# Performance work log

Hardware: AMD Instinct MI355X
Metric: run time of the kernel (lower is better)

The kernel has to match this reference:

```python
import jax, jax.numpy as jnp
import numpy as np

KH, KW = 3, 3
STRIDE = (1, 1)
PAD = (1, 1)
DIL = (1, 1)

def _unfold(x, kh, kw, stride, padding, dilation):
    # Faithful torch.nn.functional.unfold: output (B, C*kh*kw, L) with
    # feature ordering channel-slowest, then kh, then kw.
    B, C, H, W = x.shape
    h_out = (H + 2 * padding[0] - dilation[0] * (kh - 1) - 1) // stride[0] + 1
    w_out = (W + 2 * padding[1] - dilation[1] * (kw - 1) - 1) // stride[1] + 1
    xp = jnp.pad(x, ((0, 0), (0, 0), (padding[0], padding[0]), (padding[1], padding[1])))
    rows = []
    for i in range(kh):  # small fixed kernel loop (9 slices), not a data-dim loop
        for j in range(kw):
            r0 = i * dilation[0]
            c0 = j * dilation[1]
            patch = xp[:, :, r0:r0 + h_out * stride[0]:stride[0],
                             c0:c0 + w_out * stride[1]:stride[1]]  # (B,C,h_out,w_out)
            rows.append(patch)
    # stack -> (B, C, kh*kw, h_out, w_out); reorder so feature dim = C*kh*kw
    p = jnp.stack(rows, axis=2)
    p = p.reshape(B, C * kh * kw, h_out * w_out)
    return p, h_out, w_out

def transform_transposed_unfolded_input(inp_unf):
    # Default hook: identity (as in the base class).
    return inp_unf

def reference(x, weight, bias):
    B = x.shape[0]
    O = weight.shape[0]
    inp_unf, h_out, w_out = _unfold(x, KH, KW, STRIDE, PAD, DIL)   # (B, C*k*k, L)
    inp_t = jnp.swapaxes(inp_unf, 1, 2)                            # (B, L, C*k*k)
    inp_t = transform_transposed_unfolded_input(inp_t)
    w2d = weight.reshape(O, -1)                                    # (O, C*k*k)
    out_unf = jnp.einsum('blk,ok->bol', inp_t, w2d)                # (B, O, L)
    out = out_unf.reshape(B, O, h_out, w_out)
    out = out + bias.reshape(1, O, 1, 1)
    return out

def setup_inputs() -> dict:
    key = jax.random.key(0)
    k1, k2, k3 = jax.random.split(key, 3)
    x = jax.random.normal(k1, (32, 128, 56, 56), dtype=jnp.float32)
    fan_in = 128 * KH * KW
    weight = jax.random.normal(k2, (256, 128, KH, KW), dtype=jnp.float32) / np.sqrt(fan_in)
    bias = jax.random.normal(k3, (256,), dtype=jnp.float32) * 0.01
    return {"x": x, "weight": weight, "bias": bias}
```

## Files before the change

### kernel.cpp

```cpp
#include <hip/hip_runtime.h>
#include <hip/hip_bf16.h>
#include <cstdint>

typedef float f32x4 __attribute__((ext_vector_type(4)));
typedef short bf16x8 __attribute__((ext_vector_type(8)));

#define CIN   128
#define WIMG  56
#define HWSZ  3136
#define OCH   256
#define HP    58
#define WP    58
#define NT    18

__global__ void zero_border(__hip_bfloat16* __restrict__ xb) {
    int idx = blockIdx.x * 256 + threadIdx.x;
    int c8  = idx & 15;
    int t   = idx >> 4;
    int b   = t / 228;
    int pos = t - b * 228;
    int h, w;
    if (pos < 58)       { h = 0;             w = pos; }
    else if (pos < 116) { h = 57;            w = pos - 58; }
    else if (pos < 172) { h = pos - 116 + 1; w = 0; }
    else                { h = pos - 172 + 1; w = 57; }
    uint4 z = {0, 0, 0, 0};
    *(uint4*)((char*)xb + (((size_t)(b * HP + h) * WP + w) * CIN + c8 * 8) * 2) = z;
}

__global__ void cast_transpose_x(const float* __restrict__ x,
                                 __hip_bfloat16* __restrict__ xb) {
    __shared__ float tile[32][33];
    const int hw0 = blockIdx.x * 32;
    const int c0  = blockIdx.y * 32;
    const int b   = blockIdx.z;
    const int tx  = threadIdx.x;
    const int ty  = threadIdx.y;

    const float* src = x + ((size_t)(b * CIN + c0) * HWSZ) + hw0;
#pragma unroll
    for (int k = 0; k < 4; ++k) {
        int c = ty + k * 8;
        tile[c][tx] = src[(size_t)c * HWSZ + tx];
    }
    __syncthreads();
#pragma unroll
    for (int k = 0; k < 4; ++k) {
        int hwl = ty + k * 8;
        int hw = hw0 + hwl;
        int h = hw / WIMG;
        int w = hw - h * WIMG;
        size_t dst = (((size_t)b * HP + (h + 1)) * WP + (w + 1)) * CIN + c0 + tx;
        xb[dst] = __float2bfloat16(tile[tx][hwl]);
    }
}

__global__ void prep_w(const float* __restrict__ wsrc,
                       __hip_bfloat16* __restrict__ wb) {
    int idx = blockIdx.x * 256 + threadIdx.x;
    int c    = idx & 127;
    int rest = idx >> 7;
    int o    = rest & 255;
    int ij   = rest >> 8;
    wb[idx] = __float2bfloat16(wsrc[((size_t)o * CIN + c) * 9 + ij]);
}

__device__ __forceinline__ void gload16(const void* g, void* l) {
    __builtin_amdgcn_global_load_lds(
        (const __attribute__((address_space(1))) unsigned*)g,
        (__attribute__((address_space(3))) unsigned*)l,
        16, 0, 0);
}

__global__ __launch_bounds__(512, 2)
void conv_gemm(const __hip_bfloat16* __restrict__ xb,
               const __hip_bfloat16* __restrict__ wb,
               const float* __restrict__ bias,
               float* __restrict__ out) {
    extern __shared__ __attribute__((aligned(16))) char smem[];

    const int tid = threadIdx.x;
    const int wv  = tid >> 6;
    const int ln  = tid & 63;

    int bid = blockIdx.x;
    bid = (bid & 7) * 49 + (bid >> 3);
    const int m0 = bid * 256;

    const int srow = tid >> 3;
    const int cs   = tid & 7;
    const int colsrc = ((cs * 16) ^ ((srow & 7) << 4)) >> 1;
    int aOff[4], bOff[4];
#pragma unroll
    for (int q = 0; q < 4; ++q) {
        int row = q * 64 + srow;
        int p  = m0 + row;
        int b  = p / HWSZ;
        int hw = p - b * HWSZ;
        int h  = hw / WIMG;
        int w  = hw - h * WIMG;
        aOff[q] = ((b * HP + h) * WP + w) * CIN + colsrc;
        bOff[q] = row * CIN + colsrc;
    }
    const int ldsd = tid * 16;

#define SA(buf,q,offA_) gload16(xb + aOff[q] + (offA_), smem + (buf)*65536 + (q)*8192 + ldsd)
#define SB(buf,q,offB_) gload16(wb + bOff[q] + (offB_), smem + (buf)*65536 + 32768 + (q)*8192 + ldsd)

    const int wm  = wv >> 2;
    const int wn  = wv & 3;
    const int fr  = ln & 15;
    const int kby = (ln >> 4) * 16;
    const int swz = (ln & 7) << 4;

    f32x4 acc[8][4] = {};
    bf16x8 af[4][2], bq0[2][2], bq1[2][2];

#define READ_A(base, mh) do {                                                 \
    _Pragma("unroll") for (int mi = 0; mi < 4; ++mi)                          \
    _Pragma("unroll") for (int kk = 0; kk < 2; ++kk)                          \
        af[mi][kk] = *(const bf16x8*)((base) +                                \
            (wm*128 + (mh)*64 + mi*16 + fr)*128 + ((kk*64 + kby) ^ swz));     \
} while (0)

#define READ_B(base, nh, dst) do {                                            \
    _Pragma("unroll") for (int ni = 0; ni < 2; ++ni)                          \
    _Pragma("unroll") for (int kk = 0; kk < 2; ++kk)                          \
        dst[ni][kk] = *(const bf16x8*)((base) + 32768 +                       \
            (wn*64 + (nh)*32 + ni*16 + fr)*128 + ((kk*64 + kby) ^ swz));      \
} while (0)

#define MQ(mh, nh, B) do {                                                    \
    _Pragma("unroll") for (int kk = 0; kk < 2; ++kk)                          \
    _Pragma("unroll") for (int mi = 0; mi < 4; ++mi)                          \
    _Pragma("unroll") for (int ni = 0; ni < 2; ++ni)                          \
        acc[(mh)*4+mi][(nh)*2+ni] = __builtin_amdgcn_mfma_f32_16x16x32_bf16(  \
            af[mi][kk], B[ni][kk], acc[(mh)*4+mi][(nh)*2+ni], 0, 0, 0);       \
} while (0)

#define PHASE_MFMA(mh, nh, B)                                                 \
    __builtin_amdgcn_s_barrier();                                             \
    asm volatile("s_waitcnt lgkmcnt(0)" ::: "memory");                        \
    __builtin_amdgcn_s_setprio(1);                                            \
    MQ(mh, nh, B);                                                            \
    __builtin_amdgcn_s_setprio(0);                                            \
    __builtin_amdgcn_s_barrier();

    const char* base0 = smem;
    const char* base1 = smem + 65536;

    SA(0,0,0); SA(0,2,0); SB(0,0,0); SB(0,1,0); SB(0,2,0); SB(0,3,0); SA(0,1,0); SA(0,3,0);
    SA(1,0,64); SA(1,2,64);
    asm volatile("s_waitcnt vmcnt(2)" ::: "memory");
    __builtin_amdgcn_s_barrier();

#pragma unroll 1
    for (int i = 0; i < 9; ++i) {
        const int iiA = i / 3,       jjA = i - 3 * iiA;
        const int iiB = (i + 1) / 3, jjB = (i + 1) - 3 * iiB;
        const int offA1 = (iiA * WP + jjA) * CIN + 64;
        const int offB1 = i * (OCH * CIN) + 64;
        const int offA2 = (iiB * WP + jjB) * CIN;
        const int offB2 = (i + 1) * (OCH * CIN);
        const int offA3 = offA2 + 64;
        const bool pf = (i < 8);

        SB(1,0,offB1); SB(1,1,offB1);
        READ_A(base0, 0);
        READ_B(base0, 0, bq0);
        PHASE_MFMA(0, 0, bq0);

        SB(1,2,offB1); SB(1,3,offB1);
        READ_B(base0, 1, bq1);
        PHASE_MFMA(0, 1, bq1);
        asm volatile("s_waitcnt vmcnt(6)" ::: "memory");

        SA(1,1,offA1); SA(1,3,offA1);
        READ_A(base0, 1);
        PHASE_MFMA(1, 1, bq1);

        if (pf) { SA(0,0,offA2); SA(0,2,offA2); }
        __builtin_amdgcn_s_setprio(1);
        MQ(1, 0, bq0);
        __builtin_amdgcn_s_setprio(0);
        if (pf) asm volatile("s_waitcnt vmcnt(4)" ::: "memory");
        else    asm volatile("s_waitcnt vmcnt(2)" ::: "memory");
        __builtin_amdgcn_s_barrier();

        if (pf) { SB(0,0,offB2); SB(0,1,offB2); }
        READ_A(base1, 0);
        READ_B(base1, 0, bq0);
        PHASE_MFMA(0, 0, bq0);

        if (pf) { SB(0,2,offB2); SB(0,3,offB2); }
        READ_B(base1, 1, bq1);
        PHASE_MFMA(0, 1, bq1);
        if (pf) asm volatile("s_waitcnt vmcnt(6)" ::: "memory");
        else    asm volatile("s_waitcnt vmcnt(0)" ::: "memory");

        if (pf) { SA(0,1,offA2); SA(0,3,offA2); }
        READ_A(base1, 1);
        PHASE_MFMA(1, 1, bq1);

        if (pf) { SA(1,0,offA3); SA(1,2,offA3); }
        __builtin_amdgcn_s_setprio(1);
        MQ(1, 0, bq0);
        __builtin_amdgcn_s_setprio(0);
        if (pf) {
            asm volatile("s_waitcnt vmcnt(4)" ::: "memory");
            __builtin_amdgcn_s_barrier();
        }
    }
#undef SA
#undef SB
#undef READ_A
#undef READ_B
#undef MQ
#undef PHASE_MFMA

    const int laneR4 = (ln >> 4) * 4;
    float bn[4];
#pragma unroll
    for (int ni = 0; ni < 4; ++ni)
        bn[ni] = bias[wn * 64 + ni * 16 + fr];

#pragma unroll
    for (int mi = 0; mi < 8; ++mi) {
        int p0 = m0 + wm * 128 + mi * 16 + laneR4;
        int b  = p0 / HWSZ;
        int hw = p0 - b * HWSZ;
#pragma unroll
        for (int ni = 0; ni < 4; ++ni) {
            int n = wn * 64 + ni * 16 + fr;
            float4 v;
            v.x = acc[mi][ni][0] + bn[ni];
            v.y = acc[mi][ni][1] + bn[ni];
            v.z = acc[mi][ni][2] + bn[ni];
            v.w = acc[mi][ni][3] + bn[ni];
            *(float4*)(out + ((size_t)(b * OCH + n) * HWSZ + hw)) = v;
        }
    }
}

extern "C" void kernel_launch(void* const* d_in, const int* in_sizes, int n_in,
                              void* d_out, int out_size, void* d_ws, size_t ws_size,
                              hipStream_t stream) {
    const float* x    = (const float*)d_in[0];
    const float* w    = (const float*)d_in[1];
    const float* bias = (const float*)d_in[2];
    float* out = (float*)d_out;

    char* ws = (char*)d_ws;
    __hip_bfloat16* xbuf = (__hip_bfloat16*)ws;
    __hip_bfloat16* wbuf = (__hip_bfloat16*)(ws + 27557888);

    hipFuncSetAttribute(reinterpret_cast<const void*>(conv_gemm),
                        hipFuncAttributeMaxDynamicSharedMemorySize, 131072);

    zero_border<<<456, 256, 0, stream>>>(xbuf);
    cast_transpose_x<<<dim3(98, 4, 32), dim3(32, 8), 0, stream>>>(x, xbuf);
    prep_w<<<9 * 256 * 128 / 256, 256, 0, stream>>>(w, wbuf);
    conv_gemm<<<392, 512, 131072, stream>>>(xbuf, wbuf, bias, out);
}
```

Measured before the change: 104.1 us.

## Merge prep kernels, vectorize transpose stores, reorder LDS reads before global prefetch

The border-zeroing and weight-cast kernels are merged into one launch, which drops a kernel launch. The input cast/transpose now handles 64 channels per block and writes 16-byte vectors of 8 bf16 values instead of scalar stores. In the GEMM main loop, LDS fragment reads are issued before the global-to-LDS prefetches, and sched_barriers pin the order of waits and MFMA blocks. The risk is that the fixed schedule stops the compiler from interleaving instructions where that would help.

```diff
diff --git a/kernel.cpp b/kernel.cpp
--- a/kernel.cpp
+++ b/kernel.cpp
@@ -4,6 +4,7 @@
 
 typedef float f32x4 __attribute__((ext_vector_type(4)));
 typedef short bf16x8 __attribute__((ext_vector_type(8)));
+typedef short short8 __attribute__((ext_vector_type(8)));
 
 #define CIN   128
 #define WIMG  56
@@ -11,58 +12,62 @@
 #define OCH   256
 #define HP    58
 #define WP    58
-#define NT    18
-
-__global__ void zero_border(__hip_bfloat16* __restrict__ xb) {
-    int idx = blockIdx.x * 256 + threadIdx.x;
-    int c8  = idx & 15;
-    int t   = idx >> 4;
-    int b   = t / 228;
-    int pos = t - b * 228;
-    int h, w;
-    if (pos < 58)       { h = 0;             w = pos; }
-    else if (pos < 116) { h = 57;            w = pos - 58; }
-    else if (pos < 172) { h = pos - 116 + 1; w = 0; }
-    else                { h = pos - 172 + 1; w = 57; }
-    uint4 z = {0, 0, 0, 0};
-    *(uint4*)((char*)xb + (((size_t)(b * HP + h) * WP + w) * CIN + c8 * 8) * 2) = z;
-}
-
-__global__ void cast_transpose_x(const float* __restrict__ x,
-                                 __hip_bfloat16* __restrict__ xb) {
-    __shared__ float tile[32][33];
+
+__global__ void small_prep(const float* __restrict__ wsrc,
+                           __hip_bfloat16* __restrict__ wb,
+                           __hip_bfloat16* __restrict__ xb) {
+    int bidx = blockIdx.x;
+    if (bidx < 456) {
+        int idx = bidx * 256 + threadIdx.x;
+        int c8  = idx & 15;
+        int t   = idx >> 4;
+        int b   = t / 228;
+        int pos = t - b * 228;
+        int h, w;
+        if (pos < 58)       { h = 0;             w = pos; }
+        else if (pos < 116) { h = 57;            w = pos - 58; }
+        else if (pos < 172) { h = pos - 116 + 1; w = 0; }
+        else                { h = pos - 172 + 1; w = 57; }
+        uint4 z = {0, 0, 0, 0};
+        *(uint4*)((char*)xb + (((size_t)(b * HP + h) * WP + w) * CIN + c8 * 8) * 2) = z;
+    } else {
+        int idx = (bidx - 456) * 256 + threadIdx.x;
+        int c    = idx & 127;
+        int rest = idx >> 7;
+        int o    = rest & 255;
+        int ij   = rest >> 8;
+        wb[idx] = __float2bfloat16(wsrc[((size_t)o * CIN + c) * 9 + ij]);
+    }
+}
+
+__global__ __launch_bounds__(256)
+void cast_transpose_x(const float* __restrict__ x,
+                      __hip_bfloat16* __restrict__ xb) {
+    __shared__ float tile[64][33];
     const int hw0 = blockIdx.x * 32;
-    const int c0  = blockIdx.y * 32;
+    const int c0  = blockIdx.y * 64;
     const int b   = blockIdx.z;
-    const int tx  = threadIdx.x;
-    const int ty  = threadIdx.y;
-
-    const float* src = x + ((size_t)(b * CIN + c0) * HWSZ) + hw0;
-#pragma unroll
-    for (int k = 0; k < 4; ++k) {
-        int c = ty + k * 8;
-        tile[c][tx] = src[(size_t)c * HWSZ + tx];
-    }
+
+    const int lx = threadIdx.x & 31;
+    const int lc = threadIdx.x >> 5;
+    const float* src = x + ((size_t)(b * CIN + c0 + lc) * HWSZ) + hw0 + lx;
+#pragma unroll
+    for (int k = 0; k < 8; ++k)
+        tile[lc + k * 8][lx] = src[(size_t)(k * 8) * HWSZ];
     __syncthreads();
-#pragma unroll
-    for (int k = 0; k < 4; ++k) {
-        int hwl = ty + k * 8;
-        int hw = hw0 + hwl;
-        int h = hw / WIMG;
-        int w = hw - h * WIMG;
-        size_t dst = (((size_t)b * HP + (h + 1)) * WP + (w + 1)) * CIN + c0 + tx;
-        xb[dst] = __float2bfloat16(tile[tx][hwl]);
-    }
-}
-
-__global__ void prep_w(const float* __restrict__ wsrc,
-                       __hip_bfloat16* __restrict__ wb) {
-    int idx = blockIdx.x * 256 + threadIdx.x;
-    int c    = idx & 127;
-    int rest = idx >> 7;
-    int o    = rest & 255;
-    int ij   = rest >> 8;
-    wb[idx] = __float2bfloat16(wsrc[((size_t)o * CIN + c) * 9 + ij]);
+
+    const int slot = threadIdx.x & 7;
+    const int hwl  = threadIdx.x >> 3;
+    int hw = hw0 + hwl;
+    int h = hw / WIMG;
+    int w = hw - h * WIMG;
+    short8 v;
+#pragma unroll
+    for (int j = 0; j < 8; ++j) {
+        __hip_bfloat16 hb = __float2bfloat16(tile[slot * 8 + j][hwl]);
+        v[j] = *reinterpret_cast<short*>(&hb);
+    }
+    *(short8*)(xb + (((size_t)b * HP + (h + 1)) * WP + (w + 1)) * CIN + c0 + slot * 8) = v;
 }
 
 __device__ __forceinline__ void gload16(const void* g, void* l) {
@@ -138,13 +143,20 @@
             af[mi][kk], B[ni][kk], acc[(mh)*4+mi][(nh)*2+ni], 0, 0, 0);       \
 } while (0)
 
-#define PHASE_MFMA(mh, nh, B)                                                 \
+#define VMW(N) do {                                                           \
+    asm volatile("s_waitcnt vmcnt(" #N ")" ::: "memory");                     \
+    __builtin_amdgcn_sched_barrier(0);                                        \
+} while (0)
+
+#define PHASE(MQCALL) do {                                                    \
     __builtin_amdgcn_s_barrier();                                             \
     asm volatile("s_waitcnt lgkmcnt(0)" ::: "memory");                        \
+    __builtin_amdgcn_sched_barrier(0);                                        \
     __builtin_amdgcn_s_setprio(1);                                            \
-    MQ(mh, nh, B);                                                            \
+    MQCALL;                                                                   \
     __builtin_amdgcn_s_setprio(0);                                            \
-    __builtin_amdgcn_s_barrier();
+    __builtin_amdgcn_sched_barrier(0);                                        \
+} while (0)
 
     const char* base0 = smem;
     const char* base1 = smem + 65536;
@@ -165,49 +177,49 @@
         const int offA3 = offA2 + 64;
         const bool pf = (i < 8);
 
-        SB(1,0,offB1); SB(1,1,offB1);
         READ_A(base0, 0);
         READ_B(base0, 0, bq0);
-        PHASE_MFMA(0, 0, bq0);
-
+        SB(1,0,offB1); SB(1,1,offB1);
+        PHASE(MQ(0, 0, bq0));
+        __builtin_amdgcn_s_barrier();
+
+        READ_B(base0, 1, bq1);
         SB(1,2,offB1); SB(1,3,offB1);
-        READ_B(base0, 1, bq1);
-        PHASE_MFMA(0, 1, bq1);
-        asm volatile("s_waitcnt vmcnt(6)" ::: "memory");
-
+        PHASE(MQ(0, 1, bq1));
+        VMW(6);
+        __builtin_amdgcn_s_barrier();
+
+        READ_A(base0, 1);
         SA(1,1,offA1); SA(1,3,offA1);
-        READ_A(base0, 1);
-        PHASE_MFMA(1, 1, bq1);
+        PHASE(MQ(1, 1, bq1));
+        __builtin_amdgcn_s_barrier();
 
         if (pf) { SA(0,0,offA2); SA(0,2,offA2); }
-        __builtin_amdgcn_s_setprio(1);
-        MQ(1, 0, bq0);
-        __builtin_amdgcn_s_setprio(0);
-        if (pf) asm volatile("s_waitcnt vmcnt(4)" ::: "memory");
-        else    asm volatile("s_waitcnt vmcnt(2)" ::: "memory");
-        __builtin_amdgcn_s_barrier();
-
-        if (pf) { SB(0,0,offB2); SB(0,1,offB2); }
+        PHASE(MQ(1, 0, bq0));
+        if (pf) VMW(4); else VMW(2);
+        __builtin_amdgcn_s_barrier();
+
         READ_A(base1, 0);
         READ_B(base1, 0, bq0);
-        PHASE_MFMA(0, 0, bq0);
-
+        if (pf) { SB(0,0,offB2); SB(0,1,offB2); }
+        PHASE(MQ(0, 0, bq0));
+        __builtin_amdgcn_s_barrier();
+
+        READ_B(base1, 1, bq1);
         if (pf) { SB(0,2,offB2); SB(0,3,offB2); }
-        READ_B(base1, 1, bq1);
-        PHASE_MFMA(0, 1, bq1);
-        if (pf) asm volatile("s_waitcnt vmcnt(6)" ::: "memory");
-        else    asm volatile("s_waitcnt vmcnt(0)" ::: "memory");
-
+        PHASE(MQ(0, 1, bq1));
+        if (pf) VMW(6); else VMW(0);
+        __builtin_amdgcn_s_barrier();
+
+        READ_A(base1, 1);
         if (pf) { SA(0,1,offA2); SA(0,3,offA2); }
-        READ_A(base1, 1);
-        PHASE_MFMA(1, 1, bq1);
+        PHASE(MQ(1, 1, bq1));
+        __builtin_amdgcn_s_barrier();
 
         if (pf) { SA(1,0,offA3); SA(1,2,offA3); }
-        __builtin_amdgcn_s_setprio(1);
-        MQ(1, 0, bq0);
-        __builtin_amdgcn_s_setprio(0);
+        PHASE(MQ(1, 0, bq0));
         if (pf) {
-            asm volatile("s_waitcnt vmcnt(4)" ::: "memory");
+            VMW(4);
             __builtin_amdgcn_s_barrier();
         }
     }
@@ -216,7 +228,8 @@
 #undef READ_A
 #undef READ_B
 #undef MQ
-#undef PHASE_MFMA
+#undef PHASE
+#undef VMW
 
     const int laneR4 = (ln >> 4) * 4;
     float bn[4];
@@ -257,8 +270,7 @@
     hipFuncSetAttribute(reinterpret_cast<const void*>(conv_gemm),
                         hipFuncAttributeMaxDynamicSharedMemorySize, 131072);
 
-    zero_border<<<456, 256, 0, stream>>>(xbuf);
-    cast_transpose_x<<<dim3(98, 4, 32), dim3(32, 8), 0, stream>>>(x, xbuf);
-    prep_w<<<9 * 256 * 128 / 256, 256, 0, stream>>>(w, wbuf);
+    small_prep<<<1608, 256, 0, stream>>>(w, wbuf, xbuf);
+    cast_transpose_x<<<dim3(98, 2, 32), dim3(256), 0, stream>>>(x, xbuf);
     conv_gemm<<<392, 512, 131072, stream>>>(xbuf, wbuf, bias, out);
 }
```

After: 100.5 us. 1.04x faster.
